# Optimization experiments

Hardware: AMD Instinct MI355X
Metric: run time of the kernel (lower is better)

The kernel has to match this reference:

```python
import jax, jax.numpy as jnp
import numpy as np

N, H, R, C = 50000, 16, 32, 8   # nodes, hidden, relations, classes
E = 1600000                      # edges (avg degree 32)


def setup_inputs() -> dict:
    key = jax.random.key(0)
    ks = jax.random.split(key, 6)
    edge_index = jax.random.randint(ks[0], (2, E), 0, N)
    edge_type = jax.random.randint(ks[1], (E,), 0, R)
    w1 = jax.random.normal(ks[2], (R, N, H), dtype=jnp.float32) * 0.05
    root1 = jax.random.normal(ks[3], (N, H), dtype=jnp.float32) * 0.05
    b1 = jnp.zeros((H,), jnp.float32)
    w2 = jax.random.normal(ks[4], (R, H, C), dtype=jnp.float32) * 0.05
    root2 = jax.random.normal(ks[5], (H, C), dtype=jnp.float32) * 0.05
    b2 = jnp.zeros((C,), jnp.float32)
    return {"edge_index": edge_index, "edge_type": edge_type,
            "w1": w1, "root1": root1, "b1": b1,
            "w2": w2, "root2": root2, "b2": b2}


def _rel_mean_agg(msgs, dst, edge_type, num_nodes, num_rel):
    """PyG RGCNConv aggregation: mean over edges within each (relation, target)
    pair, then sum over relations. msgs: [E, d] -> [num_nodes, d]."""
    seg = edge_type * num_nodes + dst                      # combined segment id
    tot = num_rel * num_nodes
    summed = jax.ops.segment_sum(msgs, seg, num_segments=tot)      # [R*N, d]
    cnt = jax.ops.segment_sum(jnp.ones((msgs.shape[0],), msgs.dtype), seg,
                              num_segments=tot)                    # [R*N]
    mean = summed / jnp.maximum(cnt, 1.0)[:, None]
    return mean.reshape(num_rel, num_nodes, -1).sum(axis=0)       # [N, d]


def reference(edge_index, edge_type, w1, root1, b1, w2, root2, b2):
    src, dst = edge_index[0], edge_index[1]
    # ---- layer 1: x = None -> message is weight row indexed by (rel, src)
    msgs1 = w1[edge_type, src]                             # [E, H] gather
    x = _rel_mean_agg(msgs1, dst, edge_type, N, R) + root1 + b1
    x = jax.nn.relu(x)
    # ---- layer 2: precompute per-relation transforms once: [R, N, C]
    xw = jnp.einsum('nh,rhc->rnc', x, w2)
    msgs2 = xw[edge_type, src]                             # [E, C] gather
    out = _rel_mean_agg(msgs2, dst, edge_type, N, R) + x @ root2 + b2
    return jax.nn.log_softmax(out, axis=1)
```

## Files before the change

kernel.cpp:

```cpp
#include <hip/hip_runtime.h>
#include <hip/hip_bf16.h>


constexpr int Nn = 50000;
constexpr int Hh = 16;
constexpr int Rr = 32;
constexpr int Cc = 8;
constexpr int Ee = 1600000;
constexpr int CHUNK = 1024;
constexpr int NC = (Ee + CHUNK - 1) / CHUNK;
constexpr int DSH = 6;
constexpr unsigned DLOWM = 63u;
constexpr int NBKT = (Nn + 63) / 64;
constexpr int K1 = (NC + 255) / 256;
constexpr int K2 = (NBKT + 255) / 256;

__device__ __forceinline__ float b2f(__hip_bfloat16 v) { return __bfloat162float(v); }
__device__ __forceinline__ float bs2f(unsigned short u) {
    return __uint_as_float(((unsigned)u) << 16);
}

__global__ __launch_bounds__(256) void histA_kernel(const int* __restrict__ dst,
                                                    unsigned* __restrict__ H,
                                                    const unsigned short* __restrict__ w1s,
                                                    int* __restrict__ flag) {
    __shared__ unsigned hb[NBKT];
    int c = blockIdx.x, tid = threadIdx.x;
    if (c == 0 && tid == 0) {
        int hits = 0;
        for (int i = 0; i < 64; ++i) {
            unsigned short u = w1s[2 * i];
            int e = (u >> 7) & 0xFF;
            if (e >= 100 && e <= 130) ++hits;
        }
        *flag = (hits >= 32) ? 1 : 0;
    }
    for (int i = tid; i < NBKT; i += 256) hb[i] = 0;
    __syncthreads();
    int base = c * CHUNK;
    int n = min(CHUNK, Ee - base);
    for (int i = tid; i < n; i += 256)
        atomicAdd(&hb[((unsigned)dst[base + i]) >> DSH], 1u);
    __syncthreads();
    for (int i = tid; i < NBKT; i += 256) H[(size_t)c * NBKT + i] = hb[i];
}

__global__ __launch_bounds__(256) void scanB1_kernel(unsigned* __restrict__ H,
                                                     unsigned* __restrict__ bt) {
    __shared__ int lsum[4];
    int b = blockIdx.x, t = threadIdx.x, lane = t & 63, wv = t >> 6;
    int c0 = t * K1;
    int v[K1];
#pragma unroll
    for (int j = 0; j < K1; ++j) {
        int c = c0 + j;
        v[j] = (c < NC) ? (int)H[(size_t)c * NBKT + b] : 0;
    }
    int tot = 0;
#pragma unroll
    for (int j = 0; j < K1; ++j) { int tmp = v[j]; v[j] = tot; tot += tmp; }
    int s = tot;
#pragma unroll
    for (int o = 1; o < 64; o <<= 1) { int u = __shfl_up(s, o, 64); if (lane >= o) s += u; }
    if (lane == 63) lsum[wv] = s;
    __syncthreads();
    int basev = 0;
    for (int j = 0; j < wv; ++j) basev += lsum[j];
    int excl = basev + s - tot;
#pragma unroll
    for (int j = 0; j < K1; ++j) {
        int c = c0 + j;
        if (c < NC) H[(size_t)c * NBKT + b] = (unsigned)(excl + v[j]);
    }
    if (t == 255) bt[b] = (unsigned)(basev + s);
}

__global__ __launch_bounds__(256) void scanB2_kernel(const unsigned* __restrict__ bt,
                                                     unsigned* __restrict__ rbase) {
    __shared__ int lsum[4];
    int t = threadIdx.x, lane = t & 63, wv = t >> 6;
    int c0 = t * K2;
    int v[K2];
#pragma unroll
    for (int j = 0; j < K2; ++j) {
        int c = c0 + j;
        v[j] = (c < NBKT) ? (int)bt[c] : 0;
    }
    int tot = 0;
#pragma unroll
    for (int j = 0; j < K2; ++j) { int tmp = v[j]; v[j] = tot; tot += tmp; }
    int s = tot;
#pragma unroll
    for (int o = 1; o < 64; o <<= 1) { int u = __shfl_up(s, o, 64); if (lane >= o) s += u; }
    if (lane == 63) lsum[wv] = s;
    __syncthreads();
    int basev = 0;
    for (int j = 0; j < wv; ++j) basev += lsum[j];
    int excl = basev + s - tot;
#pragma unroll
    for (int j = 0; j < K2; ++j) {
        int c = c0 + j;
        if (c < NBKT) rbase[c] = (unsigned)(excl + v[j]);
    }
    if (t == 255) rbase[NBKT] = (unsigned)(basev + s);
}

__global__ __launch_bounds__(256) void scatC_kernel(const int* __restrict__ src,
                                                    const int* __restrict__ dst,
                                                    const int* __restrict__ et,
                                                    const unsigned* __restrict__ H,
                                                    const unsigned* __restrict__ rbase,
                                                    unsigned* __restrict__ rec) {
    __shared__ unsigned bb[NBKT];
    __shared__ unsigned hb[NBKT];
    int c = blockIdx.x, tid = threadIdx.x;
    for (int i = tid; i < NBKT; i += 256) {
        bb[i] = H[(size_t)c * NBKT + i] + rbase[i];
        hb[i] = 0;
    }
    __syncthreads();
    int base = c * CHUNK;
    int n = min(CHUNK, Ee - base);
    for (int i = tid; i < n; i += 256) {
        int e = base + i;
        unsigned d = (unsigned)dst[e];
        unsigned r = (unsigned)et[e];
        unsigned sv = (unsigned)src[e];
        unsigned bkt = d >> DSH;
        unsigned rank = atomicAdd(&hb[bkt], 1u);
        rec[bb[bkt] + rank] = sv | (r << 16) | ((d & DLOWM) << 21);
    }
}

__global__ __launch_bounds__(256) void sortD_kernel(const unsigned* __restrict__ rec,
                                                    const unsigned* __restrict__ rbase,
                                                    unsigned* __restrict__ sorted,
                                                    int* __restrict__ offs) {
    __shared__ unsigned cnt[64 * 33];
    __shared__ unsigned sb[64 * 33];
    int b = blockIdx.x, t = threadIdx.x;
    for (int i = t; i < 64 * 33; i += 256) cnt[i] = 0;
    __syncthreads();
    unsigned rb = rbase[b], re = rbase[b + 1];
    int n = (int)(re - rb);
    for (int i = t; i < n; i += 256) {
        unsigned w = rec[rb + i];
        atomicAdd(&cnt[((w >> 21) & 63u) * 33 + ((w >> 16) & 31u)], 1u);
    }
    __syncthreads();
    if (t < 64) {
        int deg = 0;
#pragma unroll
        for (int r = 0; r < 32; ++r) {
            unsigned cc = cnt[t * 33 + r];
            sb[t * 33 + r] = (unsigned)deg;
            deg += (int)cc;
        }
        int s = deg;
#pragma unroll
        for (int o = 1; o < 64; o <<= 1) { int u = __shfl_up(s, o, 64); if (t >= o) s += u; }
        unsigned ab = rb + (unsigned)(s - deg);
        int d = b * 64 + t;
        if (d <= Nn) offs[d] = (int)ab;
#pragma unroll
        for (int r = 0; r < 32; ++r) sb[t * 33 + r] += ab;
    }
    __syncthreads();
    for (int i = t; i < n; i += 256) {
        unsigned w = rec[rb + i];
        unsigned dlow = (w >> 21) & 63u, rel = (w >> 16) & 31u, sv = w & 0xFFFFu;
        int cell = (int)dlow * 33 + (int)rel;
        unsigned pos = atomicAdd(&sb[cell], 1u);
        unsigned cc = cnt[cell];
        if (cc > 2047u) cc = 2047u;
        sorted[pos] = sv | (rel << 16) | (cc << 21);
    }
}

__global__ __launch_bounds__(256) void l1_kernel(const unsigned* __restrict__ sorted,
                                                 const int* __restrict__ offs,
                                                 const void* __restrict__ w1,
                                                 const void* __restrict__ root1,
                                                 const void* __restrict__ b1,
                                                 const int* __restrict__ flag,
                                                 float* __restrict__ x) {
    int tid = threadIdx.x, w = tid >> 6, lane = tid & 63;
    int ep = lane >> 2, hp = lane & 3;
    int isbf = *flag;
    int d = blockIdx.x * 4 + w;
    int off = offs[d], deg = offs[d + 1] - off;
    float a0 = 0.f, a1 = 0.f, a2 = 0.f, a3 = 0.f;
    if (isbf) {
#pragma unroll 2
        for (int i = ep; i < deg; i += 16) {
            unsigned p = sorted[off + i];
            int cnt = p >> 21, rel = (p >> 16) & 31, s = p & 0xFFFF;
            float inv = __builtin_amdgcn_rcpf((float)cnt);
            ushort4 v = ((const ushort4*)w1)[((size_t)rel * Nn + s) * 4 + hp];
            a0 += inv * bs2f(v.x); a1 += inv * bs2f(v.y);
            a2 += inv * bs2f(v.z); a3 += inv * bs2f(v.w);
        }
    } else {
#pragma unroll 2
        for (int i = ep; i < deg; i += 16) {
            unsigned p = sorted[off + i];
            int cnt = p >> 21, rel = (p >> 16) & 31, s = p & 0xFFFF;
            float inv = __builtin_amdgcn_rcpf((float)cnt);
            float4 v = ((const float4*)w1)[((size_t)rel * Nn + s) * 4 + hp];
            a0 += inv * v.x; a1 += inv * v.y; a2 += inv * v.z; a3 += inv * v.w;
        }
    }
#pragma unroll
    for (int o = 4; o < 64; o <<= 1) {
        a0 += __shfl_xor(a0, o, 64);
        a1 += __shfl_xor(a1, o, 64);
        a2 += __shfl_xor(a2, o, 64);
        a3 += __shfl_xor(a3, o, 64);
    }
    if (ep == 0) {
        float r0, r1, r2, r3, bb0, bb1, bb2, bb3;
        if (isbf) {
            ushort4 rv = ((const ushort4*)root1)[(size_t)d * 4 + hp];
            ushort4 bv = ((const ushort4*)b1)[hp];
            r0 = bs2f(rv.x); r1 = bs2f(rv.y); r2 = bs2f(rv.z); r3 = bs2f(rv.w);
            bb0 = bs2f(bv.x); bb1 = bs2f(bv.y); bb2 = bs2f(bv.z); bb3 = bs2f(bv.w);
        } else {
            float4 rv = ((const float4*)root1)[(size_t)d * 4 + hp];
            float4 bv = ((const float4*)b1)[hp];
            r0 = rv.x; r1 = rv.y; r2 = rv.z; r3 = rv.w;
            bb0 = bv.x; bb1 = bv.y; bb2 = bv.z; bb3 = bv.w;
        }
        float v0 = a0 + r0 + bb0, v1 = a1 + r1 + bb1;
        float v2 = a2 + r2 + bb2, v3 = a3 + r3 + bb3;
        *(float4*)(x + (size_t)d * Hh + hp * 4) =
            make_float4(v0 > 0.f ? v0 : 0.f, v1 > 0.f ? v1 : 0.f,
                        v2 > 0.f ? v2 : 0.f, v3 > 0.f ? v3 : 0.f);
    }
}

__global__ __launch_bounds__(256) void l2_kernel(const unsigned* __restrict__ sorted,
                                                 const int* __restrict__ offs,
                                                 const float* __restrict__ x,
                                                 const void* __restrict__ w2,
                                                 const void* __restrict__ root2,
                                                 const void* __restrict__ b2v,
                                                 const int* __restrict__ flag,
                                                 void* __restrict__ out) {
    __shared__ float w2s[32 * 132];
    __shared__ float rsh[128];
    __shared__ float b2sh[8];
    int tid = threadIdx.x, w = tid >> 6, lane = tid & 63;
    int isbf = *flag;
    {
        int r = tid >> 3, cc = tid & 7;
        if (isbf) {
            const __hip_bfloat16* W = (const __hip_bfloat16*)w2 + r * 128 + cc;
#pragma unroll
            for (int h = 0; h < 16; ++h) w2s[r * 132 + cc * 16 + h] = b2f(W[h * 8]);
        } else {
            const float* W = (const float*)w2 + r * 128 + cc;
#pragma unroll
            for (int h = 0; h < 16; ++h) w2s[r * 132 + cc * 16 + h] = W[h * 8];
        }
    }
    if (tid < 128) rsh[tid] = isbf ? b2f(((const __hip_bfloat16*)root2)[tid])
                                   : ((const float*)root2)[tid];
    if (tid < 8)   b2sh[tid] = isbf ? b2f(((const __hip_bfloat16*)b2v)[tid])
                                    : ((const float*)b2v)[tid];
    __syncthreads();
    int ep = lane >> 3, c = lane & 7;
    int d = blockIdx.x * 4 + w;
    int off = offs[d], deg = offs[d + 1] - off;
    float acc = 0.0f;
    for (int i0 = 0; i0 < deg; i0 += 8) {
        int i = i0 + ep;
        if (i < deg) {
            unsigned p = sorted[off + i];
            int cnt = p >> 21, rel = (p >> 16) & 31, s = p & 0xFFFF;
            float inv = __builtin_amdgcn_rcpf((float)cnt);
            const float4* xr = (const float4*)(x + (size_t)s * Hh);
            float4 x0 = xr[0], x1 = xr[1], x2 = xr[2], x3 = xr[3];
            const float4* wv = (const float4*)(w2s + rel * 132 + c * 16);
            float4 w0 = wv[0], w1v = wv[1], w2v = wv[2], w3 = wv[3];
            float dot = x0.x*w0.x + x0.y*w0.y + x0.z*w0.z + x0.w*w0.w
                      + x1.x*w1v.x + x1.y*w1v.y + x1.z*w1v.z + x1.w*w1v.w
                      + x2.x*w2v.x + x2.y*w2v.y + x2.z*w2v.z + x2.w*w2v.w
                      + x3.x*w3.x + x3.y*w3.y + x3.z*w3.z + x3.w*w3.w;
            acc += inv * dot;
        }
    }
    acc += __shfl_xor(acc, 8, 64);
    acc += __shfl_xor(acc, 16, 64);
    acc += __shfl_xor(acc, 32, 64);
    if (ep == 0) {
        const float4* xr = (const float4*)(x + (size_t)d * Hh);
        float4 x0 = xr[0], x1 = xr[1], x2 = xr[2], x3 = xr[3];
        float xv[16] = {x0.x,x0.y,x0.z,x0.w, x1.x,x1.y,x1.z,x1.w,
                        x2.x,x2.y,x2.z,x2.w, x3.x,x3.y,x3.z,x3.w};
        float v = acc + b2sh[c];
#pragma unroll
        for (int h = 0; h < 16; ++h) v += xv[h] * rsh[h * 8 + c];
        float m = v;
#pragma unroll
        for (int o = 1; o < 8; o <<= 1) m = fmaxf(m, __shfl_xor(m, o, 8));
        float ssum = __expf(v - m);
#pragma unroll
        for (int o = 1; o < 8; o <<= 1) ssum += __shfl_xor(ssum, o, 8);
        float res = v - m - __logf(ssum);
        if (isbf) ((__hip_bfloat16*)out)[(size_t)d * Cc + c] = __float2bfloat16(res);
        else      ((float*)out)[(size_t)d * Cc + c] = res;
    }
}

extern "C" void kernel_launch(void* const* d_in, const int* in_sizes, int n_in,
                              void* d_out, int out_size, void* d_ws, size_t ws_size,
                              hipStream_t stream) {
    const int* edge_index = (const int*)d_in[0];
    const int* src = edge_index;
    const int* dst = edge_index + Ee;
    const int* et  = (const int*)d_in[1];
    const void* w1    = d_in[2];
    const void* root1 = d_in[3];
    const void* b1    = d_in[4];
    const void* w2    = d_in[5];
    const void* root2 = d_in[6];
    const void* b2    = d_in[7];

    unsigned* rec    = (unsigned*)d_ws;
    unsigned* sorted = rec + Ee;
    unsigned* H      = sorted + Ee;
    unsigned* bt     = H + (size_t)NC * NBKT;
    unsigned* rbase  = bt + NBKT;
    int* offs        = (int*)(rbase + NBKT + 1);
    int* flag        = offs + Nn + 4;
    float* x         = (float*)rec;

    histA_kernel<<<NC, 256, 0, stream>>>(dst, H, (const unsigned short*)w1, flag);
    scanB1_kernel<<<NBKT, 256, 0, stream>>>(H, bt);
    scanB2_kernel<<<1, 256, 0, stream>>>(bt, rbase);
    scatC_kernel<<<NC, 256, 0, stream>>>(src, dst, et, H, rbase, rec);
    sortD_kernel<<<NBKT, 256, 0, stream>>>(rec, rbase, sorted, offs);
    l1_kernel<<<Nn / 4, 256, 0, stream>>>(sorted, offs, w1, root1, b1, flag, x);
    l2_kernel<<<Nn / 4, 256, 0, stream>>>(sorted, offs, x, w2, root2, b2, flag, d_out);
}
```

Before: 312.4 us.

## Fuse per-bucket sort with layer-1 aggregation and stage scatter through LDS

Bucket width rises to 128 destinations and the chunk size to 4096 edges. The scatter kernel now does a local counting sort in shared memory, so its global writes to each bucket come out contiguous. The bucket sort kernel keeps the sorted records in shared memory and runs the layer-1 gather and mean directly from them, which removes a separate kernel launch and a re-read of the sorted array. The trade-off is far fewer blocks for layer 1 (about 391 instead of 12500), each running serial loops over 32 nodes per wave, which may reduce parallelism for the latency-bound gathers. A fixed 5120-entry staging buffer also assumes no bucket exceeds that size.

```diff
diff --git a/kernel.cpp b/kernel.cpp
--- a/kernel.cpp
+++ b/kernel.cpp
@@ -7,13 +7,15 @@
 constexpr int Rr = 32;
 constexpr int Cc = 8;
 constexpr int Ee = 1600000;
-constexpr int CHUNK = 1024;
+constexpr int CHUNK = 4096;
 constexpr int NC = (Ee + CHUNK - 1) / CHUNK;
-constexpr int DSH = 6;
-constexpr unsigned DLOWM = 63u;
-constexpr int NBKT = (Nn + 63) / 64;
+constexpr int DSH = 7;
+constexpr unsigned DLOWM = 127u;
+constexpr int NBKT = (Nn + 127) / 128;
 constexpr int K1 = (NC + 255) / 256;
 constexpr int K2 = (NBKT + 255) / 256;
+constexpr int KE = CHUNK / 256;
+constexpr int SCAP = 5120;
 
 __device__ __forceinline__ float b2f(__hip_bfloat16 v) { return __bfloat162float(v); }
 __device__ __forceinline__ float bs2f(unsigned short u) {
@@ -113,128 +115,174 @@
                                                     unsigned* __restrict__ rec) {
     __shared__ unsigned bb[NBKT];
     __shared__ unsigned hb[NBKT];
-    int c = blockIdx.x, tid = threadIdx.x;
-    for (int i = tid; i < NBKT; i += 256) {
+    __shared__ unsigned stg[CHUNK];
+    __shared__ unsigned short bkt16[CHUNK];
+    __shared__ int lsum[4];
+    int c = blockIdx.x, t = threadIdx.x, lane = t & 63, wv = t >> 6;
+    for (int i = t; i < NBKT; i += 256) {
         bb[i] = H[(size_t)c * NBKT + i] + rbase[i];
         hb[i] = 0;
     }
     __syncthreads();
     int base = c * CHUNK;
     int n = min(CHUNK, Ee - base);
-    for (int i = tid; i < n; i += 256) {
-        int e = base + i;
-        unsigned d = (unsigned)dst[e];
-        unsigned r = (unsigned)et[e];
-        unsigned sv = (unsigned)src[e];
-        unsigned bkt = d >> DSH;
-        unsigned rank = atomicAdd(&hb[bkt], 1u);
-        rec[bb[bkt] + rank] = sv | (r << 16) | ((d & DLOWM) << 21);
-    }
-}
-
-__global__ __launch_bounds__(256) void sortD_kernel(const unsigned* __restrict__ rec,
-                                                    const unsigned* __restrict__ rbase,
-                                                    unsigned* __restrict__ sorted,
-                                                    int* __restrict__ offs) {
-    __shared__ unsigned cnt[64 * 33];
-    __shared__ unsigned sb[64 * 33];
-    int b = blockIdx.x, t = threadIdx.x;
-    for (int i = t; i < 64 * 33; i += 256) cnt[i] = 0;
+    unsigned rcd[KE]; unsigned short bk[KE], rk[KE];
+#pragma unroll
+    for (int k = 0; k < KE; ++k) {
+        int i = t + k * 256;
+        if (i < n) {
+            int e = base + i;
+            unsigned d = (unsigned)dst[e];
+            rcd[k] = (unsigned)src[e] | ((unsigned)et[e] << 16) | ((d & DLOWM) << 21);
+            unsigned bkt = d >> DSH;
+            bk[k] = (unsigned short)bkt;
+            rk[k] = (unsigned short)atomicAdd(&hb[bkt], 1u);
+        }
+    }
+    __syncthreads();
+    {
+        int c0 = t * 2;
+        int v0 = (c0 < NBKT) ? (int)hb[c0] : 0;
+        int v1 = (c0 + 1 < NBKT) ? (int)hb[c0 + 1] : 0;
+        int pair = v0 + v1, s = pair;
+#pragma unroll
+        for (int o = 1; o < 64; o <<= 1) { int u = __shfl_up(s, o, 64); if (lane >= o) s += u; }
+        if (lane == 63) lsum[wv] = s;
+        __syncthreads();
+        int basev = 0;
+        for (int j = 0; j < wv; ++j) basev += lsum[j];
+        int excl = basev + s - pair;
+        if (c0 < NBKT) hb[c0] = (unsigned)excl;
+        if (c0 + 1 < NBKT) hb[c0 + 1] = (unsigned)(excl + v0);
+    }
+    __syncthreads();
+#pragma unroll
+    for (int k = 0; k < KE; ++k) {
+        int i = t + k * 256;
+        if (i < n) {
+            unsigned slot = hb[bk[k]] + rk[k];
+            stg[slot] = rcd[k];
+            bkt16[slot] = bk[k];
+        }
+    }
+    __syncthreads();
+    for (int i = t; i < n; i += 256) {
+        unsigned b = bkt16[i];
+        rec[bb[b] + (i - hb[b])] = stg[i];
+    }
+}
+
+__global__ __launch_bounds__(256) void sortDl1_kernel(const unsigned* __restrict__ rec,
+                                                      const unsigned* __restrict__ rbase,
+                                                      unsigned* __restrict__ sorted,
+                                                      int* __restrict__ offs,
+                                                      const void* __restrict__ w1,
+                                                      const void* __restrict__ root1,
+                                                      const void* __restrict__ b1,
+                                                      const int* __restrict__ flag,
+                                                      float* __restrict__ x) {
+    __shared__ unsigned cnt[128 * 33];
+    __shared__ unsigned sb[128 * 33];
+    __shared__ unsigned stg[SCAP];
+    __shared__ unsigned dstart[129];
+    __shared__ int l2s[2];
+    int b = blockIdx.x, t = threadIdx.x, lane = t & 63, wv = t >> 6;
+    for (int i = t; i < 128 * 33; i += 256) cnt[i] = 0;
     __syncthreads();
     unsigned rb = rbase[b], re = rbase[b + 1];
     int n = (int)(re - rb);
     for (int i = t; i < n; i += 256) {
         unsigned w = rec[rb + i];
-        atomicAdd(&cnt[((w >> 21) & 63u) * 33 + ((w >> 16) & 31u)], 1u);
-    }
-    __syncthreads();
-    if (t < 64) {
-        int deg = 0;
+        atomicAdd(&cnt[((w >> 21) & 127u) * 33 + ((w >> 16) & 31u)], 1u);
+    }
+    __syncthreads();
+    int deg = 0;
+    if (t < 128) {
 #pragma unroll
         for (int r = 0; r < 32; ++r) {
             unsigned cc = cnt[t * 33 + r];
             sb[t * 33 + r] = (unsigned)deg;
             deg += (int)cc;
         }
-        int s = deg;
-#pragma unroll
-        for (int o = 1; o < 64; o <<= 1) { int u = __shfl_up(s, o, 64); if (t >= o) s += u; }
-        unsigned ab = rb + (unsigned)(s - deg);
-        int d = b * 64 + t;
-        if (d <= Nn) offs[d] = (int)ab;
-#pragma unroll
-        for (int r = 0; r < 32; ++r) sb[t * 33 + r] += ab;
+    }
+    int s = deg;
+#pragma unroll
+    for (int o = 1; o < 64; o <<= 1) { int u = __shfl_up(s, o, 64); if (lane >= o) s += u; }
+    if (lane == 63 && wv < 2) l2s[wv] = s;
+    __syncthreads();
+    if (t < 128) {
+        int excl = s - deg + (wv == 1 ? l2s[0] : 0);
+        dstart[t] = (unsigned)excl;
+        if (t == 127) dstart[128] = (unsigned)(excl + deg);
+        int d = b * 128 + t;
+        if (d <= Nn) offs[d] = (int)(rb + (unsigned)excl);
+#pragma unroll
+        for (int r = 0; r < 32; ++r) sb[t * 33 + r] += (unsigned)excl;
     }
     __syncthreads();
     for (int i = t; i < n; i += 256) {
         unsigned w = rec[rb + i];
-        unsigned dlow = (w >> 21) & 63u, rel = (w >> 16) & 31u, sv = w & 0xFFFFu;
+        unsigned dlow = (w >> 21) & 127u, rel = (w >> 16) & 31u, sv = w & 0xFFFFu;
         int cell = (int)dlow * 33 + (int)rel;
         unsigned pos = atomicAdd(&sb[cell], 1u);
         unsigned cc = cnt[cell];
         if (cc > 2047u) cc = 2047u;
-        sorted[pos] = sv | (rel << 16) | (cc << 21);
-    }
-}
-
-__global__ __launch_bounds__(256) void l1_kernel(const unsigned* __restrict__ sorted,
-                                                 const int* __restrict__ offs,
-                                                 const void* __restrict__ w1,
-                                                 const void* __restrict__ root1,
-                                                 const void* __restrict__ b1,
-                                                 const int* __restrict__ flag,
-                                                 float* __restrict__ x) {
-    int tid = threadIdx.x, w = tid >> 6, lane = tid & 63;
+        stg[pos] = sv | (rel << 16) | (cc << 21);
+    }
+    __syncthreads();
+    for (int i = t; i < n; i += 256) sorted[rb + i] = stg[i];
+    int isbf = *flag;
     int ep = lane >> 2, hp = lane & 3;
-    int isbf = *flag;
-    int d = blockIdx.x * 4 + w;
-    int off = offs[d], deg = offs[d + 1] - off;
-    float a0 = 0.f, a1 = 0.f, a2 = 0.f, a3 = 0.f;
-    if (isbf) {
-#pragma unroll 2
-        for (int i = ep; i < deg; i += 16) {
-            unsigned p = sorted[off + i];
-            int cnt = p >> 21, rel = (p >> 16) & 31, s = p & 0xFFFF;
-            float inv = __builtin_amdgcn_rcpf((float)cnt);
-            ushort4 v = ((const ushort4*)w1)[((size_t)rel * Nn + s) * 4 + hp];
-            a0 += inv * bs2f(v.x); a1 += inv * bs2f(v.y);
-            a2 += inv * bs2f(v.z); a3 += inv * bs2f(v.w);
-        }
-    } else {
-#pragma unroll 2
-        for (int i = ep; i < deg; i += 16) {
-            unsigned p = sorted[off + i];
-            int cnt = p >> 21, rel = (p >> 16) & 31, s = p & 0xFFFF;
-            float inv = __builtin_amdgcn_rcpf((float)cnt);
-            float4 v = ((const float4*)w1)[((size_t)rel * Nn + s) * 4 + hp];
-            a0 += inv * v.x; a1 += inv * v.y; a2 += inv * v.z; a3 += inv * v.w;
-        }
-    }
-#pragma unroll
-    for (int o = 4; o < 64; o <<= 1) {
-        a0 += __shfl_xor(a0, o, 64);
-        a1 += __shfl_xor(a1, o, 64);
-        a2 += __shfl_xor(a2, o, 64);
-        a3 += __shfl_xor(a3, o, 64);
-    }
-    if (ep == 0) {
-        float r0, r1, r2, r3, bb0, bb1, bb2, bb3;
+    for (int j = 0; j < 32; ++j) {
+        int dl = wv * 32 + j;
+        int d = b * 128 + dl;
+        if (d >= Nn) break;
+        int s0 = (int)dstart[dl], s1 = (int)dstart[dl + 1];
+        float a0 = 0.f, a1 = 0.f, a2 = 0.f, a3 = 0.f;
         if (isbf) {
-            ushort4 rv = ((const ushort4*)root1)[(size_t)d * 4 + hp];
-            ushort4 bv = ((const ushort4*)b1)[hp];
-            r0 = bs2f(rv.x); r1 = bs2f(rv.y); r2 = bs2f(rv.z); r3 = bs2f(rv.w);
-            bb0 = bs2f(bv.x); bb1 = bs2f(bv.y); bb2 = bs2f(bv.z); bb3 = bs2f(bv.w);
+            for (int i = s0 + ep; i < s1; i += 16) {
+                unsigned p = stg[i];
+                int ct = p >> 21, rel = (p >> 16) & 31, sv = p & 0xFFFF;
+                float inv = __builtin_amdgcn_rcpf((float)ct);
+                ushort4 v = ((const ushort4*)w1)[((size_t)rel * Nn + sv) * 4 + hp];
+                a0 += inv * bs2f(v.x); a1 += inv * bs2f(v.y);
+                a2 += inv * bs2f(v.z); a3 += inv * bs2f(v.w);
+            }
         } else {
-            float4 rv = ((const float4*)root1)[(size_t)d * 4 + hp];
-            float4 bv = ((const float4*)b1)[hp];
-            r0 = rv.x; r1 = rv.y; r2 = rv.z; r3 = rv.w;
-            bb0 = bv.x; bb1 = bv.y; bb2 = bv.z; bb3 = bv.w;
-        }
-        float v0 = a0 + r0 + bb0, v1 = a1 + r1 + bb1;
-        float v2 = a2 + r2 + bb2, v3 = a3 + r3 + bb3;
-        *(float4*)(x + (size_t)d * Hh + hp * 4) =
-            make_float4(v0 > 0.f ? v0 : 0.f, v1 > 0.f ? v1 : 0.f,
-                        v2 > 0.f ? v2 : 0.f, v3 > 0.f ? v3 : 0.f);
+            for (int i = s0 + ep; i < s1; i += 16) {
+                unsigned p = stg[i];
+                int ct = p >> 21, rel = (p >> 16) & 31, sv = p & 0xFFFF;
+                float inv = __builtin_amdgcn_rcpf((float)ct);
+                float4 v = ((const float4*)w1)[((size_t)rel * Nn + sv) * 4 + hp];
+                a0 += inv * v.x; a1 += inv * v.y; a2 += inv * v.z; a3 += inv * v.w;
+            }
+        }
+#pragma unroll
+        for (int o = 4; o < 64; o <<= 1) {
+            a0 += __shfl_xor(a0, o, 64);
+            a1 += __shfl_xor(a1, o, 64);
+            a2 += __shfl_xor(a2, o, 64);
+            a3 += __shfl_xor(a3, o, 64);
+        }
+        if (ep == 0) {
+            float r0, r1, r2, r3, bb0, bb1, bb2, bb3;
+            if (isbf) {
+                ushort4 rv = ((const ushort4*)root1)[(size_t)d * 4 + hp];
+                ushort4 bv = ((const ushort4*)b1)[hp];
+                r0 = bs2f(rv.x); r1 = bs2f(rv.y); r2 = bs2f(rv.z); r3 = bs2f(rv.w);
+                bb0 = bs2f(bv.x); bb1 = bs2f(bv.y); bb2 = bs2f(bv.z); bb3 = bs2f(bv.w);
+            } else {
+                float4 rv = ((const float4*)root1)[(size_t)d * 4 + hp];
+                float4 bv = ((const float4*)b1)[hp];
+                r0 = rv.x; r1 = rv.y; r2 = rv.z; r3 = rv.w;
+                bb0 = bv.x; bb1 = bv.y; bb2 = bv.z; bb3 = bv.w;
+            }
+            float v0 = a0 + r0 + bb0, v1 = a1 + r1 + bb1;
+            float v2 = a2 + r2 + bb2, v3 = a3 + r3 + bb3;
+            *(float4*)(x + (size_t)d * Hh + hp * 4) =
+                make_float4(v0 > 0.f ? v0 : 0.f, v1 > 0.f ? v1 : 0.f,
+                            v2 > 0.f ? v2 : 0.f, v3 > 0.f ? v3 : 0.f);
+        }
     }
 }
 
@@ -328,18 +376,18 @@
 
     unsigned* rec    = (unsigned*)d_ws;
     unsigned* sorted = rec + Ee;
-    unsigned* H      = sorted + Ee;
+    float*    x      = (float*)(sorted + Ee);
+    unsigned* H      = (unsigned*)(x + (size_t)Nn * Hh);
     unsigned* bt     = H + (size_t)NC * NBKT;
     unsigned* rbase  = bt + NBKT;
     int* offs        = (int*)(rbase + NBKT + 1);
     int* flag        = offs + Nn + 4;
-    float* x         = (float*)rec;
 
     histA_kernel<<<NC, 256, 0, stream>>>(dst, H, (const unsigned short*)w1, flag);
     scanB1_kernel<<<NBKT, 256, 0, stream>>>(H, bt);
     scanB2_kernel<<<1, 256, 0, stream>>>(bt, rbase);
     scatC_kernel<<<NC, 256, 0, stream>>>(src, dst, et, H, rbase, rec);
-    sortD_kernel<<<NBKT, 256, 0, stream>>>(rec, rbase, sorted, offs);
-    l1_kernel<<<Nn / 4, 256, 0, stream>>>(sorted, offs, w1, root1, b1, flag, x);
+    sortDl1_kernel<<<NBKT, 256, 0, stream>>>(rec, rbase, sorted, offs,
+                                             w1, root1, b1, flag, x);
     l2_kernel<<<Nn / 4, 256, 0, stream>>>(sorted, offs, x, w2, root2, b2, flag, d_out);
 }
```

New measurement: 316.4 us. About the same (+1.3%).
